# Performance work log

Hardware: AMD Instinct MI355X
Metric: run time of the kernel (lower is better)

Reference implementation:

```python
import jax, jax.numpy as jnp
import numpy as np

FEATURE_MAP = 1024
DIM = 1024
SEQ_LEN = 128
BATCH = 128
WINDOW = 5


def setup_inputs() -> dict:
    key = jax.random.key(0)
    k1, k2 = jax.random.split(key)
    x = jax.random.normal(k1, (BATCH, SEQ_LEN, DIM), dtype=jnp.float32)
    # xavier-uniform-ish scale for Ws
    limit = np.sqrt(6.0 / (DIM + FEATURE_MAP)).astype(np.float32)
    Ws = jax.random.uniform(k2, (WINDOW, DIM, FEATURE_MAP), dtype=jnp.float32,
                            minval=-limit, maxval=limit)
    b = jnp.zeros((FEATURE_MAP,), dtype=jnp.float32)
    return {"x": x, "Ws": Ws, "b": b}


def reference(x, Ws, b):
    # x: [B, L, D] batch-first -> work in time-major order like the original.
    # Precompute all 5 projections for every timestep in one big einsum:
    # proj: [L, W, B, F]
    proj = jnp.einsum('bld,wdf->lwbf', x, Ws)
    B = x.shape[0]
    h0 = jnp.zeros((WINDOW, B, FEATURE_MAP), dtype=x.dtype)

    def step(h, p):
        # h, p: [W, B, F]
        # m1 = max(p0, h1); m_k = max(h_{k-1} + p_k, h_k) for k>=2 (old h used)
        cand = jnp.concatenate([p[:1], h[:-1] + p[1:]], axis=0)
        new_h = jnp.maximum(cand, h)
        return new_h, None

    h_final, _ = jax.lax.scan(step, h0, proj)
    return jnp.tanh(h_final[WINDOW - 1] + b[None, :])  # [B, F]
```

## Files before the change

kernel.cpp:

```cpp
#include <hip/hip_runtime.h>
#include <hip/hip_bf16.h>

#define WINDOW 5
#define DIM 1024
#define FEAT 1024
#define SEQ 128
#define BATCH 128
#define MTOT (BATCH*SEQ)
#define NTOT (WINDOW*FEAT)
#define KTOT 1024

#define DCHUNK 16

typedef int int4v __attribute__((ext_vector_type(4)));

static __device__ __forceinline__ unsigned short f2bf(float f) {
  union { float f; unsigned int i; } c; c.f = f;
  unsigned int i = c.i;
  unsigned int lsb = (i >> 16) & 1u;
  i += 0x7fffu + lsb;
  return (unsigned short)(i >> 16);
}
static __device__ __forceinline__ float bf2f(unsigned short u) {
  union { unsigned int i; float f; } c; c.i = ((unsigned int)u) << 16; return c.f;
}
static __device__ __forceinline__ signed char q8(float v, float inv) {
  float q = rintf(v * inv);
  q = fminf(fmaxf(q, -127.f), 127.f);
  return (signed char)(int)q;
}

__global__ __launch_bounds__(256) void quant_x(const float* __restrict__ x,
                                               signed char* __restrict__ xq,
                                               float* __restrict__ sx) {
  int row  = blockIdx.x * 4 + (threadIdx.x >> 6);
  int lane = threadIdx.x & 63;
  const float* xr = x + (size_t)row * KTOT;

  float4 v[4];
  float amax = 0.f;
  #pragma unroll
  for (int i = 0; i < 4; i++) {
    v[i] = ((const float4*)xr)[i * 64 + lane];
    amax = fmaxf(amax, fmaxf(fmaxf(fabsf(v[i].x), fabsf(v[i].y)),
                             fmaxf(fabsf(v[i].z), fabsf(v[i].w))));
  }
  #pragma unroll
  for (int m = 1; m < 64; m <<= 1)
    amax = fmaxf(amax, __shfl_xor(amax, m));

  float inv = amax > 0.f ? 127.f / amax : 0.f;
  int* xqr = (int*)(xq + (size_t)row * KTOT);
  #pragma unroll
  for (int i = 0; i < 4; i++) {
    int p = ((int)(unsigned char)q8(v[i].x, inv)) |
            ((int)(unsigned char)q8(v[i].y, inv) << 8) |
            ((int)(unsigned char)q8(v[i].z, inv) << 16) |
            ((int)q8(v[i].w, inv) << 24);
    xqr[i * 64 + lane] = p;
  }
  if (lane == 0) sx[row] = amax / 127.f;
}

__global__ __launch_bounds__(256) void w_colamax_part(const float* __restrict__ Ws,
                                                      float* __restrict__ part) {
  int w  = blockIdx.z;
  int dc = blockIdx.y;
  int f4 = threadIdx.x;
  const float* p = Ws + ((size_t)w * DIM + (size_t)dc * DCHUNK) * FEAT;
  float4 m = {0.f, 0.f, 0.f, 0.f};
  #pragma unroll
  for (int d = 0; d < DCHUNK; d++) {
    float4 v = ((const float4*)(p + (size_t)d * FEAT))[f4];
    m.x = fmaxf(m.x, fabsf(v.x));
    m.y = fmaxf(m.y, fabsf(v.y));
    m.z = fmaxf(m.z, fabsf(v.z));
    m.w = fmaxf(m.w, fabsf(v.w));
  }
  ((float4*)(part + ((size_t)w * (DIM / DCHUNK) + dc) * FEAT))[f4] = m;
}

__global__ __launch_bounds__(256) void w_colamax_reduce(const float* __restrict__ part,
                                                        float* __restrict__ sw) {
  int idx = blockIdx.x * 256 + threadIdx.x;
  int w = idx >> 10, f = idx & 1023;
  const float* p = part + (size_t)w * (DIM / DCHUNK) * FEAT + f;
  float m = 0.f;
  #pragma unroll 8
  for (int c = 0; c < DIM / DCHUNK; c++)
    m = fmaxf(m, p[(size_t)c * FEAT]);
  sw[idx] = m / 127.f;
}

__global__ __launch_bounds__(256) void transq_ws(const float* __restrict__ Ws,
                                                 const float* __restrict__ sw,
                                                 signed char* __restrict__ wq) {
  __shared__ float tile[32][33];
  int w  = blockIdx.z;
  int f0 = blockIdx.x * 32, d0 = blockIdx.y * 32;
  int tx = threadIdx.x, ty = threadIdx.y;
  const float* src = Ws + ((size_t)w * DIM + d0) * FEAT + f0;
  #pragma unroll
  for (int i = 0; i < 4; i++)
    tile[ty + 8*i][tx] = src[(size_t)(ty + 8*i) * FEAT + tx];
  __syncthreads();
  signed char* dst = wq + ((size_t)w * FEAT + f0) * DIM + d0;
  #pragma unroll
  for (int i = 0; i < 4; i++) {
    int f = f0 + ty + 8*i;
    float swv = sw[(w << 10) + f];
    float inv = swv > 0.f ? 1.0f / swv : 0.f;
    dst[(size_t)(ty + 8*i) * DIM + tx] = q8(tile[tx][ty + 8*i], inv);
  }
}

__global__ __launch_bounds__(256, 3) void fused_gemm_scan(
    const signed char* __restrict__ xq,
    const signed char* __restrict__ wq,
    const float* __restrict__ sx,
    const float* __restrict__ swp,
    const float* __restrict__ bias,
    float* __restrict__ out)
{
  __shared__ __align__(16) char smem[40960];
  signed char* As = (signed char*)smem;
  signed char* Bs = (signed char*)(smem + 16384);

  const int tid  = threadIdx.x;
  const int wid  = tid >> 6;
  const int lane = tid & 63;

  int bid = blockIdx.x;
  int wg  = ((bid & 7) << 9) + (bid >> 3);
  const int b  = wg >> 5;
  const int f0 = (wg & 31) << 5;

  const signed char* aG = xq + (size_t)b * SEQ * KTOT;

  const int wm = wid >> 1, wn = wid & 1;
  const int rowin = lane >> 3;
  const int swb16 = ((lane & 7) ^ rowin) << 4;

  int4v acc[4][5];
  #pragma unroll
  for (int i = 0; i < 4; i++)
    #pragma unroll
    for (int j = 0; j < 5; j++)
      acc[i][j] = (int4v){0, 0, 0, 0};

  for (int kt = 0; kt < 8; kt++) {
    const int k0 = kt << 7;
    #pragma unroll
    for (int c = 0; c < 9; c++) {
      int seg = wid * 9 + c;
      if (seg < 16) {
        int row = (seg << 3) + rowin;
        __builtin_amdgcn_global_load_lds(
            (const __attribute__((address_space(1))) void*)(aG + (size_t)row * KTOT + k0 + swb16),
            (__attribute__((address_space(3))) void*)(As + (seg << 10)), 16, 0, 0);
      } else {
        int sb = seg - 16;
        int r  = (sb << 3) + rowin;
        const signed char* src = wq
            + ((size_t)(((r >> 5) << 10) + f0 + (r & 31))) * KTOT + k0 + swb16;
        __builtin_amdgcn_global_load_lds(
            (const __attribute__((address_space(1))) void*)src,
            (__attribute__((address_space(3))) void*)(Bs + (sb << 10)), 16, 0, 0);
      }
    }
    __syncthreads();

    #pragma unroll
    for (int kk = 0; kk < 2; kk++) {
      int4v a[4], bf[5];
      #pragma unroll
      for (int i = 0; i < 4; i++) {
        int row  = wm * 64 + i * 16 + (lane & 15);
        int slot = (lane >> 4) + (kk << 2);
        a[i] = *(const int4v*)(As + row * 128 + ((slot ^ (row & 7)) << 4));
      }
      #pragma unroll
      for (int j = 0; j < 5; j++) {
        int row  = wn * 80 + j * 16 + (lane & 15);
        int slot = (lane >> 4) + (kk << 2);
        bf[j] = *(const int4v*)(Bs + row * 128 + ((slot ^ (row & 7)) << 4));
      }
      #pragma unroll
      for (int i = 0; i < 4; i++)
        #pragma unroll
        for (int j = 0; j < 5; j++)
          acc[i][j] = __builtin_amdgcn_mfma_i32_16x16x64_i8(a[i], bf[j], acc[i][j], 0, 0, 0);
    }
    __syncthreads();
  }

  float sxv[16];
  #pragma unroll
  for (int i = 0; i < 4; i++)
    #pragma unroll
    for (int r = 0; r < 4; r++)
      sxv[i * 4 + r] = sx[b * SEQ + wm * 64 + i * 16 + ((lane >> 4) << 2) + r];
  float swv[5];
  #pragma unroll
  for (int j = 0; j < 5; j++) {
    int c = wn * 80 + j * 16 + (lane & 15);
    swv[j] = swp[((c >> 5) << 10) + f0 + (c & 31)];
  }

  #pragma unroll
  for (int i = 0; i < 4; i++) {
    #pragma unroll
    for (int j = 0; j < 5; j++) {
      #pragma unroll
      for (int r = 0; r < 4; r++) {
        int l = wm * 64 + i * 16 + ((lane >> 4) << 2) + r;
        int c = wn * 80 + j * 16 + (lane & 15);
        float v = (float)acc[i][j][r] * sxv[i * 4 + r] * swv[j];
        int byte = ((l * 160 + c) << 1) ^ (((l >> 2) & 3) << 5);
        *(unsigned short*)(smem + byte) = f2bf(v);
      }
    }
  }
  __syncthreads();

  if (tid < 32) {
    const int f = tid;
    float h0 = 0.f, h1 = 0.f, h2 = 0.f, h3 = 0.f, h4 = 0.f;
    for (int l = 0; l < SEQ; l++) {
      const int swz  = ((l >> 2) & 3) << 5;
      const int base = l * 320;
      float p[5];
      #pragma unroll
      for (int w = 0; w < 5; w++) {
        int byte = (base + (((w << 5) + f) << 1)) ^ swz;
        p[w] = bf2f(*(const unsigned short*)(smem + byte));
      }
      h4 = fmaxf(h3 + p[4], h4);
      h3 = fmaxf(h2 + p[3], h3);
      h2 = fmaxf(h1 + p[2], h2);
      h1 = fmaxf(h0 + p[1], h1);
      h0 = fmaxf(p[0], h0);
    }
    out[b * FEAT + f0 + f] = tanhf(h4 + bias[f0 + f]);
  }
}

extern "C" void kernel_launch(void* const* d_in, const int* in_sizes, int n_in,
                              void* d_out, int out_size, void* d_ws, size_t ws_size,
                              hipStream_t stream) {
  const float* x  = (const float*)d_in[0];
  const float* Ws = (const float*)d_in[1];
  const float* b  = (const float*)d_in[2];
  float* out = (float*)d_out;

  char* ws = (char*)d_ws;
  const size_t XQ_BYTES = (size_t)MTOT * KTOT;
  const size_t WQ_BYTES = (size_t)WINDOW * FEAT * DIM;
  const size_t SX_BYTES = (size_t)MTOT * 4;
  const size_t SW_BYTES = (size_t)WINDOW * FEAT * 4;
  signed char* xq = (signed char*)ws;
  signed char* wq = (signed char*)(ws + XQ_BYTES);
  float* sx   = (float*)(ws + XQ_BYTES + WQ_BYTES);
  float* sw   = (float*)(ws + XQ_BYTES + WQ_BYTES + SX_BYTES);
  float* part = (float*)(ws + XQ_BYTES + WQ_BYTES + SX_BYTES + SW_BYTES);

  hipLaunchKernelGGL(quant_x, dim3(MTOT / 4), dim3(256), 0, stream, x, xq, sx);
  hipLaunchKernelGGL(w_colamax_part, dim3(1, DIM / DCHUNK, WINDOW), dim3(256), 0, stream,
                     Ws, part);
  hipLaunchKernelGGL(w_colamax_reduce, dim3(NTOT / 256), dim3(256), 0, stream, part, sw);
  hipLaunchKernelGGL(transq_ws, dim3(FEAT / 32, DIM / 32, WINDOW), dim3(32, 8), 0, stream,
                     Ws, sw, wq);
  hipLaunchKernelGGL(fused_gemm_scan, dim3(BATCH * 32), dim3(256), 0, stream,
                     xq, wq, sx, sw, b, out);
}
```

Baseline: 175.4 us.

## Double-buffer int8 GEMM K-loop with async global-to-LDS prefetch

Replaces the single-buffered K loop with a two-stage LDS ping-pong. The next K tile is loaded with global_load_lds while MFMAs consume the current one, paced by explicit vmcnt waits, s_barrier and sched_barrier. Load pointers and swizzled LDS offsets are precomputed per wave so the loop carries less address arithmetic. The larger shared-memory footprint means launch bounds drop from 3 to 2 blocks per CU, trading occupancy for overlap of memory latency.

Result: slower. 226.7 us (+29.2%).

```diff
diff --git a/kernel.cpp b/kernel.cpp
--- a/kernel.cpp
+++ b/kernel.cpp
@@ -11,6 +11,7 @@
 #define KTOT 1024
 
 #define DCHUNK 16
+#define BUFB 36864
 
 typedef int int4v __attribute__((ext_vector_type(4)));
 
@@ -114,7 +115,7 @@
   }
 }
 
-__global__ __launch_bounds__(256, 3) void fused_gemm_scan(
+__global__ __launch_bounds__(256, 2) void fused_gemm_scan(
     const signed char* __restrict__ xq,
     const signed char* __restrict__ wq,
     const float* __restrict__ sx,
@@ -122,9 +123,7 @@
     const float* __restrict__ bias,
     float* __restrict__ out)
 {
-  __shared__ __align__(16) char smem[40960];
-  signed char* As = (signed char*)smem;
-  signed char* Bs = (signed char*)(smem + 16384);
+  __shared__ __align__(16) char smem[2 * BUFB];
 
   const int tid  = threadIdx.x;
   const int wid  = tid >> 6;
@@ -135,11 +134,50 @@
   const int b  = wg >> 5;
   const int f0 = (wg & 31) << 5;
 
-  const signed char* aG = xq + (size_t)b * SEQ * KTOT;
-
   const int wm = wid >> 1, wn = wid & 1;
   const int rowin = lane >> 3;
   const int swb16 = ((lane & 7) ^ rowin) << 4;
+
+  const char* pA = (const char*)xq + ((size_t)b * SEQ + wid * 32 + rowin) * KTOT + swb16;
+  const char* pB0, *pB1, *pB2, *pB3, *pB4;
+  {
+    int r0 = wid * 40 + rowin;
+    #define BPTR(c_) ((const char*)wq + \
+        (size_t)((((r0 + 8*(c_)) >> 5) << 10) + f0 + ((r0 + 8*(c_)) & 31)) * KTOT + swb16)
+    pB0 = BPTR(0); pB1 = BPTR(1); pB2 = BPTR(2); pB3 = BPTR(3); pB4 = BPTR(4);
+    #undef BPTR
+  }
+  const int dstA = wid * 4096;
+  const int dstB = 16384 + wid * 5120;
+
+  #define AS1 __attribute__((address_space(1)))
+  #define AS3 __attribute__((address_space(3)))
+  #define STAGE(koff_, bufoff_) do {                                               \
+    __builtin_amdgcn_global_load_lds((const AS1 void*)(pA + (koff_)),              \
+        (AS3 void*)(smem + (bufoff_) + dstA),        16, 0, 0);                    \
+    __builtin_amdgcn_global_load_lds((const AS1 void*)(pA + 8192 + (koff_)),       \
+        (AS3 void*)(smem + (bufoff_) + dstA + 1024), 16, 0, 0);                    \
+    __builtin_amdgcn_global_load_lds((const AS1 void*)(pA + 16384 + (koff_)),      \
+        (AS3 void*)(smem + (bufoff_) + dstA + 2048), 16, 0, 0);                    \
+    __builtin_amdgcn_global_load_lds((const AS1 void*)(pA + 24576 + (koff_)),      \
+        (AS3 void*)(smem + (bufoff_) + dstA + 3072), 16, 0, 0);                    \
+    __builtin_amdgcn_global_load_lds((const AS1 void*)(pB0 + (koff_)),             \
+        (AS3 void*)(smem + (bufoff_) + dstB),        16, 0, 0);                    \
+    __builtin_amdgcn_global_load_lds((const AS1 void*)(pB1 + (koff_)),             \
+        (AS3 void*)(smem + (bufoff_) + dstB + 1024), 16, 0, 0);                    \
+    __builtin_amdgcn_global_load_lds((const AS1 void*)(pB2 + (koff_)),             \
+        (AS3 void*)(smem + (bufoff_) + dstB + 2048), 16, 0, 0);                    \
+    __builtin_amdgcn_global_load_lds((const AS1 void*)(pB3 + (koff_)),             \
+        (AS3 void*)(smem + (bufoff_) + dstB + 3072), 16, 0, 0);                    \
+    __builtin_amdgcn_global_load_lds((const AS1 void*)(pB4 + (koff_)),             \
+        (AS3 void*)(smem + (bufoff_) + dstB + 4096), 16, 0, 0);                    \
+  } while (0)
+
+  const int r7   = (lane & 15) & 7;
+  const int sx0o = (((lane >> 4) + 0) ^ r7) << 4;
+  const int sx1o = (((lane >> 4) + 4) ^ r7) << 4;
+  const int rA128 = (wm * 64 + (lane & 15)) * 128;
+  const int rB128 = (wn * 80 + (lane & 15)) * 128;
 
   int4v acc[4][5];
   #pragma unroll
@@ -148,51 +186,69 @@
     for (int j = 0; j < 5; j++)
       acc[i][j] = (int4v){0, 0, 0, 0};
 
-  for (int kt = 0; kt < 8; kt++) {
-    const int k0 = kt << 7;
-    #pragma unroll
-    for (int c = 0; c < 9; c++) {
-      int seg = wid * 9 + c;
-      if (seg < 16) {
-        int row = (seg << 3) + rowin;
-        __builtin_amdgcn_global_load_lds(
-            (const __attribute__((address_space(1))) void*)(aG + (size_t)row * KTOT + k0 + swb16),
-            (__attribute__((address_space(3))) void*)(As + (seg << 10)), 16, 0, 0);
-      } else {
-        int sb = seg - 16;
-        int r  = (sb << 3) + rowin;
-        const signed char* src = wq
-            + ((size_t)(((r >> 5) << 10) + f0 + (r & 31))) * KTOT + k0 + swb16;
-        __builtin_amdgcn_global_load_lds(
-            (const __attribute__((address_space(1))) void*)src,
-            (__attribute__((address_space(3))) void*)(Bs + (sb << 10)), 16, 0, 0);
-      }
-    }
-    __syncthreads();
-
-    #pragma unroll
-    for (int kk = 0; kk < 2; kk++) {
-      int4v a[4], bf[5];
-      #pragma unroll
-      for (int i = 0; i < 4; i++) {
-        int row  = wm * 64 + i * 16 + (lane & 15);
-        int slot = (lane >> 4) + (kk << 2);
-        a[i] = *(const int4v*)(As + row * 128 + ((slot ^ (row & 7)) << 4));
-      }
-      #pragma unroll
-      for (int j = 0; j < 5; j++) {
-        int row  = wn * 80 + j * 16 + (lane & 15);
-        int slot = (lane >> 4) + (kk << 2);
-        bf[j] = *(const int4v*)(Bs + row * 128 + ((slot ^ (row & 7)) << 4));
-      }
-      #pragma unroll
-      for (int i = 0; i < 4; i++)
-        #pragma unroll
-        for (int j = 0; j < 5; j++)
-          acc[i][j] = __builtin_amdgcn_mfma_i32_16x16x64_i8(a[i], bf[j], acc[i][j], 0, 0, 0);
-    }
-    __syncthreads();
-  }
+  #define COMPUTE(bufoff_) do {                                                    \
+    int4v a_[4], b_[5];                                                            \
+    _Pragma("unroll")                                                              \
+    for (int i = 0; i < 4; i++)                                                    \
+      a_[i] = *(const int4v*)(smem + (bufoff_) + rA128 + sx0o + i * 2048);         \
+    _Pragma("unroll")                                                              \
+    for (int j = 0; j < 5; j++)                                                    \
+      b_[j] = *(const int4v*)(smem + (bufoff_) + 16384 + rB128 + sx0o + j * 2048); \
+    _Pragma("unroll")                                                              \
+    for (int i = 0; i < 4; i++)                                                    \
+      _Pragma("unroll")                                                            \
+      for (int j = 0; j < 5; j++)                                                  \
+        acc[i][j] = __builtin_amdgcn_mfma_i32_16x16x64_i8(a_[i], b_[j], acc[i][j], 0, 0, 0); \
+    _Pragma("unroll")                                                              \
+    for (int i = 0; i < 4; i++)                                                    \
+      a_[i] = *(const int4v*)(smem + (bufoff_) + rA128 + sx1o + i * 2048);         \
+    _Pragma("unroll")                                                              \
+    for (int j = 0; j < 5; j++)                                                    \
+      b_[j] = *(const int4v*)(smem + (bufoff_) + 16384 + rB128 + sx1o + j * 2048); \
+    _Pragma("unroll")                                                              \
+    for (int i = 0; i < 4; i++)                                                    \
+      _Pragma("unroll")                                                            \
+      for (int j = 0; j < 5; j++)                                                  \
+        acc[i][j] = __builtin_amdgcn_mfma_i32_16x16x64_i8(a_[i], b_[j], acc[i][j], 0, 0, 0); \
+  } while (0)
+
+  #define SB __builtin_amdgcn_sched_barrier(0)
+
+  STAGE(0, 0);
+  STAGE(128, BUFB);
+  pA += 256; pB0 += 256; pB1 += 256; pB2 += 256; pB3 += 256; pB4 += 256;
+
+  for (int kt2 = 0; kt2 < 3; kt2++) {
+    asm volatile("s_waitcnt vmcnt(9)" ::: "memory");
+    __builtin_amdgcn_s_barrier();
+    SB;
+    COMPUTE(0);
+    SB;
+    __builtin_amdgcn_s_barrier();
+    SB;
+    STAGE(0, 0);
+    asm volatile("s_waitcnt vmcnt(9)" ::: "memory");
+    __builtin_amdgcn_s_barrier();
+    SB;
+    COMPUTE(BUFB);
+    SB;
+    __builtin_amdgcn_s_barrier();
+    SB;
+    STAGE(128, BUFB);
+    pA += 256; pB0 += 256; pB1 += 256; pB2 += 256; pB3 += 256; pB4 += 256;
+  }
+  asm volatile("s_waitcnt vmcnt(9)" ::: "memory");
+  __builtin_amdgcn_s_barrier();
+  SB;
+  COMPUTE(0);
+  SB;
+  __builtin_amdgcn_s_barrier();
+  asm volatile("s_waitcnt vmcnt(0)" ::: "memory");
+  __builtin_amdgcn_s_barrier();
+  SB;
+  COMPUTE(BUFB);
+
+  __syncthreads();
 
   float sxv[16];
   #pragma unroll
@@ -243,6 +299,11 @@
     }
     out[b * FEAT + f0 + f] = tanhf(h4 + bias[f0 + f]);
   }
+  #undef STAGE
+  #undef COMPUTE
+  #undef SB
+  #undef AS1
+  #undef AS3
 }
 
 extern "C" void kernel_launch(void* const* d_in, const int* in_sizes, int n_in,
```

## Load GEMM fragments directly from global into registers, transpose scan buffer

Applied to the files above, without the earlier changes.

Replaces the LDS-staged int8 GEMM (global_load_lds plus barriers) with per-lane direct global loads of MFMA fragments into double-buffered registers, removing LDS traffic and the two __syncthreads per k-tile. The scan staging buffer is re-laid out feature-major with a padded stride so each scan thread reads 8 timesteps per 16-byte vector load instead of scalar loads. Launch bounds drop to 2 blocks per SM to allow the larger register footprint. The cost is redundant global/L2 reads, since fragments are no longer shared across waves through LDS, and reduced occupancy.

Result: slower. 341.0 us (+94.4%).

```diff
diff --git a/kernel.cpp b/kernel.cpp
--- a/kernel.cpp
+++ b/kernel.cpp
@@ -11,6 +11,7 @@
 #define KTOT 1024
 
 #define DCHUNK 16
+#define PSTRIDE 272
 
 typedef int int4v __attribute__((ext_vector_type(4)));
 
@@ -114,7 +115,7 @@
   }
 }
 
-__global__ __launch_bounds__(256, 3) void fused_gemm_scan(
+__global__ __launch_bounds__(256, 2) void fused_gemm_scan(
     const signed char* __restrict__ xq,
     const signed char* __restrict__ wq,
     const float* __restrict__ sx,
@@ -122,9 +123,7 @@
     const float* __restrict__ bias,
     float* __restrict__ out)
 {
-  __shared__ __align__(16) char smem[40960];
-  signed char* As = (signed char*)smem;
-  signed char* Bs = (signed char*)(smem + 16384);
+  __shared__ __align__(16) char smem[160 * PSTRIDE];
 
   const int tid  = threadIdx.x;
   const int wid  = tid >> 6;
@@ -135,11 +134,19 @@
   const int b  = wg >> 5;
   const int f0 = (wg & 31) << 5;
 
-  const signed char* aG = xq + (size_t)b * SEQ * KTOT;
-
   const int wm = wid >> 1, wn = wid & 1;
-  const int rowin = lane >> 3;
-  const int swb16 = ((lane & 7) ^ rowin) << 4;
+  const int kslot = (lane >> 4) << 4;
+
+  const signed char* aP[4];
+  #pragma unroll
+  for (int i = 0; i < 4; i++)
+    aP[i] = xq + ((size_t)(b * SEQ + wm * 64 + i * 16 + (lane & 15))) * KTOT + kslot;
+  const signed char* bP[5];
+  #pragma unroll
+  for (int j = 0; j < 5; j++) {
+    int c = wn * 80 + j * 16 + (lane & 15);
+    bP[j] = wq + ((size_t)(((c >> 5) << 10) + f0 + (c & 31))) * KTOT + kslot;
+  }
 
   int4v acc[4][5];
   #pragma unroll
@@ -148,50 +155,29 @@
     for (int j = 0; j < 5; j++)
       acc[i][j] = (int4v){0, 0, 0, 0};
 
-  for (int kt = 0; kt < 8; kt++) {
-    const int k0 = kt << 7;
-    #pragma unroll
-    for (int c = 0; c < 9; c++) {
-      int seg = wid * 9 + c;
-      if (seg < 16) {
-        int row = (seg << 3) + rowin;
-        __builtin_amdgcn_global_load_lds(
-            (const __attribute__((address_space(1))) void*)(aG + (size_t)row * KTOT + k0 + swb16),
-            (__attribute__((address_space(3))) void*)(As + (seg << 10)), 16, 0, 0);
-      } else {
-        int sb = seg - 16;
-        int r  = (sb << 3) + rowin;
-        const signed char* src = wq
-            + ((size_t)(((r >> 5) << 10) + f0 + (r & 31))) * KTOT + k0 + swb16;
-        __builtin_amdgcn_global_load_lds(
-            (const __attribute__((address_space(1))) void*)src,
-            (__attribute__((address_space(3))) void*)(Bs + (sb << 10)), 16, 0, 0);
-      }
+  int4v fa[2][4], fb[2][5];
+  #pragma unroll
+  for (int i = 0; i < 4; i++) fa[0][i] = *(const int4v*)(aP[i]);
+  #pragma unroll
+  for (int j = 0; j < 5; j++) fb[0][j] = *(const int4v*)(bP[j]);
+
+  #pragma unroll
+  for (int s = 0; s < 16; s++) {
+    const int cur = s & 1, nxt = cur ^ 1;
+    if (s < 15) {
+      #pragma unroll
+      for (int i = 0; i < 4; i++)
+        fa[nxt][i] = *(const int4v*)(aP[i] + (s + 1) * 64);
+      #pragma unroll
+      for (int j = 0; j < 5; j++)
+        fb[nxt][j] = *(const int4v*)(bP[j] + (s + 1) * 64);
     }
-    __syncthreads();
-
-    #pragma unroll
-    for (int kk = 0; kk < 2; kk++) {
-      int4v a[4], bf[5];
-      #pragma unroll
-      for (int i = 0; i < 4; i++) {
-        int row  = wm * 64 + i * 16 + (lane & 15);
-        int slot = (lane >> 4) + (kk << 2);
-        a[i] = *(const int4v*)(As + row * 128 + ((slot ^ (row & 7)) << 4));
-      }
-      #pragma unroll
-      for (int j = 0; j < 5; j++) {
-        int row  = wn * 80 + j * 16 + (lane & 15);
-        int slot = (lane >> 4) + (kk << 2);
-        bf[j] = *(const int4v*)(Bs + row * 128 + ((slot ^ (row & 7)) << 4));
-      }
-      #pragma unroll
-      for (int i = 0; i < 4; i++)
-        #pragma unroll
-        for (int j = 0; j < 5; j++)
-          acc[i][j] = __builtin_amdgcn_mfma_i32_16x16x64_i8(a[i], bf[j], acc[i][j], 0, 0, 0);
-    }
-    __syncthreads();
+    #pragma unroll
+    for (int i = 0; i < 4; i++)
+      #pragma unroll
+      for (int j = 0; j < 5; j++)
+        acc[i][j] = __builtin_amdgcn_mfma_i32_16x16x64_i8(fa[cur][i], fb[cur][j],
+                                                          acc[i][j], 0, 0, 0);
   }
 
   float sxv[16];
@@ -211,37 +197,42 @@
   for (int i = 0; i < 4; i++) {
     #pragma unroll
     for (int j = 0; j < 5; j++) {
+      const int c  = wn * 80 + j * 16 + (lane & 15);
+      const int pr = (c & 31) * 5 + (c >> 5);
       #pragma unroll
       for (int r = 0; r < 4; r++) {
         int l = wm * 64 + i * 16 + ((lane >> 4) << 2) + r;
-        int c = wn * 80 + j * 16 + (lane & 15);
         float v = (float)acc[i][j][r] * sxv[i * 4 + r] * swv[j];
-        int byte = ((l * 160 + c) << 1) ^ (((l >> 2) & 3) << 5);
-        *(unsigned short*)(smem + byte) = f2bf(v);
+        *(unsigned short*)(smem + pr * PSTRIDE + l * 2) = f2bf(v);
       }
     }
   }
   __syncthreads();
 
   if (tid < 32) {
-    const int f = tid;
+    const int fl = tid;
     float h0 = 0.f, h1 = 0.f, h2 = 0.f, h3 = 0.f, h4 = 0.f;
-    for (int l = 0; l < SEQ; l++) {
-      const int swz  = ((l >> 2) & 3) << 5;
-      const int base = l * 320;
-      float p[5];
-      #pragma unroll
-      for (int w = 0; w < 5; w++) {
-        int byte = (base + (((w << 5) + f) << 1)) ^ swz;
-        p[w] = bf2f(*(const unsigned short*)(smem + byte));
+    for (int lc = 0; lc < 16; lc++) {
+      int4v pw[5];
+      #pragma unroll
+      for (int w = 0; w < 5; w++)
+        pw[w] = *(const int4v*)(smem + (fl * 5 + w) * PSTRIDE + lc * 16);
+      #pragma unroll
+      for (int e = 0; e < 8; e++) {
+        float p[5];
+        #pragma unroll
+        for (int w = 0; w < 5; w++) {
+          unsigned int u = ((const unsigned int*)&pw[w])[e >> 1];
+          p[w] = bf2f((unsigned short)((e & 1) ? (u >> 16) : (u & 0xffffu)));
+        }
+        h4 = fmaxf(h3 + p[4], h4);
+        h3 = fmaxf(h2 + p[3], h3);
+        h2 = fmaxf(h1 + p[2], h2);
+        h1 = fmaxf(h0 + p[1], h1);
+        h0 = fmaxf(p[0], h0);
       }
-      h4 = fmaxf(h3 + p[4], h4);
-      h3 = fmaxf(h2 + p[3], h3);
-      h2 = fmaxf(h1 + p[2], h2);
-      h1 = fmaxf(h0 + p[1], h1);
-      h0 = fmaxf(p[0], h0);
     }
-    out[b * FEAT + f0 + f] = tanhf(h4 + bias[f0 + f]);
+    out[b * FEAT + f0 + fl] = tanhf(h4 + bias[f0 + fl]);
   }
 }
 
```

## Use 512-thread blocks, transpose projection staging for vectorized scan reads

Applied to the files above, without the earlier changes.

Doubles the fused GEMM+scan block to 8 waves, so each wave computes a 32x80 tile instead of 64x80. This halves the accumulators per thread and spreads the global-to-LDS loads over more waves. The projection tile is now staged in LDS transposed (feature-window rows, time contiguous, padded stride, XOR swizzle). Writes become packed 8-byte stores and the serial scan threads read 16-byte vectors covering 8 timesteps. The risk is that the larger LDS footprint and block size lower the number of resident blocks, and the scan is still done by only 32 threads.

After: 189.8 us. +8.2%, slower.

```diff
diff --git a/kernel.cpp b/kernel.cpp
--- a/kernel.cpp
+++ b/kernel.cpp
@@ -11,8 +11,10 @@
 #define KTOT 1024
 
 #define DCHUNK 16
+#define PSTRIDE 272
 
 typedef int int4v __attribute__((ext_vector_type(4)));
+typedef short short4v __attribute__((ext_vector_type(4)));
 
 static __device__ __forceinline__ unsigned short f2bf(float f) {
   union { float f; unsigned int i; } c; c.f = f;
@@ -114,7 +116,7 @@
   }
 }
 
-__global__ __launch_bounds__(256, 3) void fused_gemm_scan(
+__global__ __launch_bounds__(512, 4) void fused_gemm_scan(
     const signed char* __restrict__ xq,
     const signed char* __restrict__ wq,
     const float* __restrict__ sx,
@@ -122,7 +124,7 @@
     const float* __restrict__ bias,
     float* __restrict__ out)
 {
-  __shared__ __align__(16) char smem[40960];
+  __shared__ __align__(16) char smem[160 * PSTRIDE];
   signed char* As = (signed char*)smem;
   signed char* Bs = (signed char*)(smem + 16384);
 
@@ -141,65 +143,82 @@
   const int rowin = lane >> 3;
   const int swb16 = ((lane & 7) ^ rowin) << 4;
 
-  int4v acc[4][5];
-  #pragma unroll
-  for (int i = 0; i < 4; i++)
+  const int l7   = lane & 7;
+  const int sx0o = (((lane >> 4) + 0) ^ l7) << 4;
+  const int sx1o = (((lane >> 4) + 4) ^ l7) << 4;
+
+  int4v acc[2][5];
+  #pragma unroll
+  for (int i = 0; i < 2; i++)
     #pragma unroll
     for (int j = 0; j < 5; j++)
       acc[i][j] = (int4v){0, 0, 0, 0};
 
+  #define AS1 __attribute__((address_space(1)))
+  #define AS3 __attribute__((address_space(3)))
+
   for (int kt = 0; kt < 8; kt++) {
     const int k0 = kt << 7;
     #pragma unroll
-    for (int c = 0; c < 9; c++) {
-      int seg = wid * 9 + c;
-      if (seg < 16) {
-        int row = (seg << 3) + rowin;
-        __builtin_amdgcn_global_load_lds(
-            (const __attribute__((address_space(1))) void*)(aG + (size_t)row * KTOT + k0 + swb16),
-            (__attribute__((address_space(3))) void*)(As + (seg << 10)), 16, 0, 0);
-      } else {
-        int sb = seg - 16;
+    for (int c = 0; c < 2; c++) {
+      int seg = wid * 2 + c;
+      int row = (seg << 3) + rowin;
+      __builtin_amdgcn_global_load_lds(
+          (const AS1 void*)(aG + (size_t)row * KTOT + k0 + swb16),
+          (AS3 void*)(As + (seg << 10)), 16, 0, 0);
+    }
+    if (wid < 4) {
+      #pragma unroll
+      for (int c = 0; c < 3; c++) {
+        int sb = wid * 3 + c;
         int r  = (sb << 3) + rowin;
         const signed char* src = wq
             + ((size_t)(((r >> 5) << 10) + f0 + (r & 31))) * KTOT + k0 + swb16;
         __builtin_amdgcn_global_load_lds(
-            (const __attribute__((address_space(1))) void*)src,
-            (__attribute__((address_space(3))) void*)(Bs + (sb << 10)), 16, 0, 0);
+            (const AS1 void*)src, (AS3 void*)(Bs + (sb << 10)), 16, 0, 0);
+      }
+    } else {
+      #pragma unroll
+      for (int c = 0; c < 2; c++) {
+        int sb = 12 + (wid - 4) * 2 + c;
+        int r  = (sb << 3) + rowin;
+        const signed char* src = wq
+            + ((size_t)(((r >> 5) << 10) + f0 + (r & 31))) * KTOT + k0 + swb16;
+        __builtin_amdgcn_global_load_lds(
+            (const AS1 void*)src, (AS3 void*)(Bs + (sb << 10)), 16, 0, 0);
       }
     }
     __syncthreads();
 
     #pragma unroll
     for (int kk = 0; kk < 2; kk++) {
-      int4v a[4], bf[5];
-      #pragma unroll
-      for (int i = 0; i < 4; i++) {
-        int row  = wm * 64 + i * 16 + (lane & 15);
-        int slot = (lane >> 4) + (kk << 2);
-        a[i] = *(const int4v*)(As + row * 128 + ((slot ^ (row & 7)) << 4));
+      const int so = kk ? sx1o : sx0o;
+      int4v a_[2], b_[5];
+      #pragma unroll
+      for (int i = 0; i < 2; i++) {
+        int row = wm * 32 + i * 16 + (lane & 15);
+        a_[i] = *(const int4v*)(As + row * 128 + so);
       }
       #pragma unroll
       for (int j = 0; j < 5; j++) {
-        int row  = wn * 80 + j * 16 + (lane & 15);
-        int slot = (lane >> 4) + (kk << 2);
-        bf[j] = *(const int4v*)(Bs + row * 128 + ((slot ^ (row & 7)) << 4));
-      }
-      #pragma unroll
-      for (int i = 0; i < 4; i++)
+        int row = wn * 80 + j * 16 + (lane & 15);
+        b_[j] = *(const int4v*)(Bs + row * 128 + so);
+      }
+      #pragma unroll
+      for (int i = 0; i < 2; i++)
         #pragma unroll
         for (int j = 0; j < 5; j++)
-          acc[i][j] = __builtin_amdgcn_mfma_i32_16x16x64_i8(a[i], bf[j], acc[i][j], 0, 0, 0);
+          acc[i][j] = __builtin_amdgcn_mfma_i32_16x16x64_i8(a_[i], b_[j], acc[i][j], 0, 0, 0);
     }
     __syncthreads();
   }
 
-  float sxv[16];
-  #pragma unroll
-  for (int i = 0; i < 4; i++)
+  float sxv[8];
+  #pragma unroll
+  for (int i = 0; i < 2; i++)
     #pragma unroll
     for (int r = 0; r < 4; r++)
-      sxv[i * 4 + r] = sx[b * SEQ + wm * 64 + i * 16 + ((lane >> 4) << 2) + r];
+      sxv[i * 4 + r] = sx[b * SEQ + wm * 32 + i * 16 + ((lane >> 4) << 2) + r];
   float swv[5];
   #pragma unroll
   for (int j = 0; j < 5; j++) {
@@ -208,17 +227,18 @@
   }
 
   #pragma unroll
-  for (int i = 0; i < 4; i++) {
+  for (int i = 0; i < 2; i++) {
+    const int l0 = wm * 32 + i * 16 + ((lane >> 4) << 2);
     #pragma unroll
     for (int j = 0; j < 5; j++) {
-      #pragma unroll
-      for (int r = 0; r < 4; r++) {
-        int l = wm * 64 + i * 16 + ((lane >> 4) << 2) + r;
-        int c = wn * 80 + j * 16 + (lane & 15);
-        float v = (float)acc[i][j][r] * sxv[i * 4 + r] * swv[j];
-        int byte = ((l * 160 + c) << 1) ^ (((l >> 2) & 3) << 5);
-        *(unsigned short*)(smem + byte) = f2bf(v);
-      }
+      const int c   = wn * 80 + j * 16 + (lane & 15);
+      const int row = (c & 31) * 5 + (c >> 5);
+      short4v pack;
+      #pragma unroll
+      for (int r = 0; r < 4; r++)
+        pack[r] = (short)f2bf((float)acc[i][j][r] * sxv[i * 4 + r] * swv[j]);
+      int byte = (row * PSTRIDE + l0 * 2) ^ ((row & 7) << 4);
+      *(short4v*)(smem + byte) = pack;
     }
   }
   __syncthreads();
@@ -226,23 +246,34 @@
   if (tid < 32) {
     const int f = tid;
     float h0 = 0.f, h1 = 0.f, h2 = 0.f, h3 = 0.f, h4 = 0.f;
-    for (int l = 0; l < SEQ; l++) {
-      const int swz  = ((l >> 2) & 3) << 5;
-      const int base = l * 320;
-      float p[5];
+    #pragma unroll
+    for (int lc = 0; lc < 16; lc++) {
+      int4v pw[5];
       #pragma unroll
       for (int w = 0; w < 5; w++) {
-        int byte = (base + (((w << 5) + f) << 1)) ^ swz;
-        p[w] = bf2f(*(const unsigned short*)(smem + byte));
-      }
-      h4 = fmaxf(h3 + p[4], h4);
-      h3 = fmaxf(h2 + p[3], h3);
-      h2 = fmaxf(h1 + p[2], h2);
-      h1 = fmaxf(h0 + p[1], h1);
-      h0 = fmaxf(p[0], h0);
+        int row  = f * 5 + w;
+        int byte = (row * PSTRIDE + lc * 16) ^ ((row & 7) << 4);
+        pw[w] = *(const int4v*)(smem + byte);
+      }
+      #pragma unroll
+      for (int e = 0; e < 8; e++) {
+        float p[5];
+        #pragma unroll
+        for (int w = 0; w < 5; w++) {
+          unsigned int u = ((const unsigned int*)&pw[w])[e >> 1];
+          p[w] = bf2f((unsigned short)((e & 1) ? (u >> 16) : (u & 0xffffu)));
+        }
+        h4 = fmaxf(h3 + p[4], h4);
+        h3 = fmaxf(h2 + p[3], h3);
+        h2 = fmaxf(h1 + p[2], h2);
+        h1 = fmaxf(h0 + p[1], h1);
+        h0 = fmaxf(p[0], h0);
+      }
     }
     out[b * FEAT + f0 + f] = tanhf(h4 + bias[f0 + f]);
   }
+  #undef AS1
+  #undef AS3
 }
 
 extern "C" void kernel_launch(void* const* d_in, const int* in_sizes, int n_in,
@@ -270,6 +301,6 @@
   hipLaunchKernelGGL(w_colamax_reduce, dim3(NTOT / 256), dim3(256), 0, stream, part, sw);
   hipLaunchKernelGGL(transq_ws, dim3(FEAT / 32, DIM / 32, WINDOW), dim3(32, 8), 0, stream,
                      Ws, sw, wq);
-  hipLaunchKernelGGL(fused_gemm_scan, dim3(BATCH * 32), dim3(256), 0, stream,
+  hipLaunchKernelGGL(fused_gemm_scan, dim3(BATCH * 32), dim3(512), 0, stream,
                      xq, wq, sx, sw, b, out);
 }
```
